# Performance work log

Measured on AMD Instinct MI355X. Metric: run time of the kernel, lower is better.

The kernel has to match this reference:

```python
import jax, jax.numpy as jnp
import numpy as np

VOCAB = 50000
COVOCAB = 50000
D = 300
NUM_SENSES = 4
B = 100000


def _xavier(key, shape):
    fan_in, fan_out = shape[-2], shape[-1]
    if len(shape) == 3:
        fan_in, fan_out = shape[1], shape[2]
    limit = (6.0 / (fan_in + fan_out)) ** 0.5
    return jax.random.uniform(key, shape, jnp.float32, -limit, limit)


def setup_inputs() -> dict:
    key = jax.random.key(0)
    k1, k2, k3, k4, k5 = jax.random.split(key, 5)
    V = _xavier(k1, (VOCAB, D, NUM_SENSES))
    W = _xavier(k2, (COVOCAB, D, NUM_SENSES))
    vb = _xavier(k3, (VOCAB, NUM_SENSES))
    wb = _xavier(k4, (COVOCAB, NUM_SENSES))
    IJ = jax.random.randint(k5, (B, 2), 0, VOCAB, dtype=jnp.int64)
    return {"V": V, "W": W, "vb": vb, "wb": wb, "IJ": IJ}


def reference(V, W, vb, wb, IJ):
    i = IJ[:, 0]
    j = IJ[:, 1]
    Vg = V[i]            # [B, d, s_v]  gather
    Wg = W[j]            # [B, d, s_w]  gather
    # bmm(W[j]^T, V[i]) -> [B, s_w, s_v]
    mat = jnp.einsum("bds,bdt->bst", Wg, Vg)
    bias = wb[j][:, :, None] + vb[i][:, None, :]   # [B, s_w, s_v]
    mat = mat + bias
    # faithful to original: log(sum(exp(.)))
    return jnp.log(jnp.sum(jnp.exp(mat), axis=(1, 2)))
```

## Files before the change

kernel.cpp:

```cpp
#include <hip/hip_runtime.h>
#include <hip/hip_bf16.h>


constexpr int D   = 300;
constexpr int NS  = 4;
constexpr int ROW = D * NS;

__global__ __launch_bounds__(256) void multisense_kernel(
    const float* __restrict__ V,
    const float* __restrict__ W,
    const float* __restrict__ vb,
    const float* __restrict__ wb,
    const unsigned int* __restrict__ IJw,
    float* __restrict__ out,
    int B)
{
    const int lane = threadIdx.x & 63;
    const int b    = blockIdx.x * (blockDim.x >> 6) + (threadIdx.x >> 6);
    if (b >= B) return;

    unsigned int probe = (lane < 32) ? IJw[2 * lane + 1] : 0u;
    const bool isI64 = (__ballot(probe != 0u) == 0ull);

    int i, j;
    if (isI64) { i = (int)IJw[4 * (size_t)b];     j = (int)IJw[4 * (size_t)b + 2]; }
    else       { i = (int)IJw[2 * (size_t)b];     j = (int)IJw[2 * (size_t)b + 1]; }

    const float* __restrict__ Vr = V + (size_t)i * ROW;
    const float* __restrict__ Wr = W + (size_t)j * ROW;

    const int s_idx = (lane >> 4) & 3;
    const int t_idx = (lane >> 2) & 3;

    const float wbj = wb[(size_t)j * NS + s_idx];
    const float vbi = vb[(size_t)i * NS + t_idx];

    float4 va[5], wa[5];
#pragma unroll
    for (int k = 0; k < 4; ++k) {
        const int d = lane + 64 * k;
        va[k] = *reinterpret_cast<const float4*>(Vr + (size_t)d * NS);
        wa[k] = *reinterpret_cast<const float4*>(Wr + (size_t)d * NS);
    }
    {
        const int  d4 = 256 + lane;
        const int  dc = (d4 < D) ? d4 : 0;
        const float m = (d4 < D) ? 1.0f : 0.0f;
        va[4] = *reinterpret_cast<const float4*>(Vr + (size_t)dc * NS);
        wa[4] = *reinterpret_cast<const float4*>(Wr + (size_t)dc * NS);
        wa[4].x *= m; wa[4].y *= m; wa[4].z *= m; wa[4].w *= m;
    }

    float acc[16];
#pragma unroll
    for (int m = 0; m < 16; ++m) acc[m] = 0.0f;
#pragma unroll
    for (int k = 0; k < 5; ++k) {
        const float v0 = va[k].x, v1 = va[k].y, v2 = va[k].z, v3 = va[k].w;
        const float w0 = wa[k].x, w1 = wa[k].y, w2 = wa[k].z, w3 = wa[k].w;
        acc[ 0] = fmaf(w0, v0, acc[ 0]); acc[ 1] = fmaf(w0, v1, acc[ 1]);
        acc[ 2] = fmaf(w0, v2, acc[ 2]); acc[ 3] = fmaf(w0, v3, acc[ 3]);
        acc[ 4] = fmaf(w1, v0, acc[ 4]); acc[ 5] = fmaf(w1, v1, acc[ 5]);
        acc[ 6] = fmaf(w1, v2, acc[ 6]); acc[ 7] = fmaf(w1, v3, acc[ 7]);
        acc[ 8] = fmaf(w2, v0, acc[ 8]); acc[ 9] = fmaf(w2, v1, acc[ 9]);
        acc[10] = fmaf(w2, v2, acc[10]); acc[11] = fmaf(w2, v3, acc[11]);
        acc[12] = fmaf(w3, v0, acc[12]); acc[13] = fmaf(w3, v1, acc[13]);
        acc[14] = fmaf(w3, v2, acc[14]); acc[15] = fmaf(w3, v3, acc[15]);
    }

    const bool b5 = (lane & 32) != 0;
    float r8[8];
#pragma unroll
    for (int m = 0; m < 8; ++m) {
        const float send = b5 ? acc[m]     : acc[m + 8];
        const float keep = b5 ? acc[m + 8] : acc[m];
        r8[m] = keep + __shfl_xor(send, 32, 64);
    }
    const bool b4 = (lane & 16) != 0;
    float r4[4];
#pragma unroll
    for (int m = 0; m < 4; ++m) {
        const float send = b4 ? r8[m]     : r8[m + 4];
        const float keep = b4 ? r8[m + 4] : r8[m];
        r4[m] = keep + __shfl_xor(send, 16, 64);
    }
    const bool b3 = (lane & 8) != 0;
    float r2[2];
#pragma unroll
    for (int m = 0; m < 2; ++m) {
        const float send = b3 ? r4[m]     : r4[m + 2];
        const float keep = b3 ? r4[m + 2] : r4[m];
        r2[m] = keep + __shfl_xor(send, 8, 64);
    }
    const bool b2 = (lane & 4) != 0;
    float r1;
    {
        const float send = b2 ? r2[0] : r2[1];
        const float keep = b2 ? r2[1] : r2[0];
        r1 = keep + __shfl_xor(send, 4, 64);
    }
    r1 += __shfl_xor(r1, 2, 64);
    r1 += __shfl_xor(r1, 1, 64);

    float e = expf(r1 + wbj + vbi);
    e += __shfl_xor(e,  4, 64);
    e += __shfl_xor(e,  8, 64);
    e += __shfl_xor(e, 16, 64);
    e += __shfl_xor(e, 32, 64);

    if (lane == 0) out[b] = logf(e);
}

extern "C" void kernel_launch(void* const* d_in, const int* in_sizes, int n_in,
                              void* d_out, int out_size, void* d_ws, size_t ws_size,
                              hipStream_t stream) {
    const float* V  = (const float*)d_in[0];
    const float* W  = (const float*)d_in[1];
    const float* vb = (const float*)d_in[2];
    const float* wb = (const float*)d_in[3];
    const unsigned int* IJ = (const unsigned int*)d_in[4];
    float* out = (float*)d_out;

    const int B = out_size;
    const int wavesPerBlock = 4;
    dim3 block(256);
    dim3 grid((B + wavesPerBlock - 1) / wavesPerBlock);
    hipLaunchKernelGGL(multisense_kernel, grid, block, 0, stream,
                       V, W, vb, wb, IJ, out, B);
}
```

Baseline: 510.4 us.

## Software-pipeline gathers with persistent waves and inline-asm double-buffered loads

Replaces the one-wave-per-row launch with a persistent grid of 1024 blocks, where each wave walks rows with a grid stride. Each wave prefetches the next row's V/W slices, biases and the index pair after next into a second register set while it computes the current row. Explicit vmcnt waits and sched barriers hold this order. The goal is to hide gather latency, which matters because each row is latency-bound with little work, at the cost of more registers and fragile hand-counted waitcnts. It also picks the index width on the host from the input size instead of probing.

```diff
diff --git a/kernel.cpp b/kernel.cpp
--- a/kernel.cpp
+++ b/kernel.cpp
@@ -1,10 +1,102 @@
 #include <hip/hip_runtime.h>
-#include <hip/hip_bf16.h>
-
-
-constexpr int D   = 300;
-constexpr int NS  = 4;
-constexpr int ROW = D * NS;
+
+
+typedef __attribute__((ext_vector_type(4))) float f32x4;
+
+constexpr int D    = 300;
+constexpr int NS   = 4;
+constexpr int ROWB = D * NS * 4;
+
+#define S_VMCNT(N) asm volatile("s_waitcnt vmcnt(" #N ")" ::: "memory")
+
+#define STAGE(NV, NW, pV_, pW_, pVt_, pWt_)                                                  \
+    asm volatile("global_load_dwordx4 %0, %1, off"             : "=v"(NV[0]) : "v"(pV_));    \
+    asm volatile("global_load_dwordx4 %0, %1, off offset:1024" : "=v"(NV[1]) : "v"(pV_));    \
+    asm volatile("global_load_dwordx4 %0, %1, off offset:2048" : "=v"(NV[2]) : "v"(pV_));    \
+    asm volatile("global_load_dwordx4 %0, %1, off offset:3072" : "=v"(NV[3]) : "v"(pV_));    \
+    asm volatile("global_load_dwordx4 %0, %1, off"             : "=v"(NV[4]) : "v"(pVt_));   \
+    asm volatile("global_load_dwordx4 %0, %1, off"             : "=v"(NW[0]) : "v"(pW_));    \
+    asm volatile("global_load_dwordx4 %0, %1, off offset:1024" : "=v"(NW[1]) : "v"(pW_));    \
+    asm volatile("global_load_dwordx4 %0, %1, off offset:2048" : "=v"(NW[2]) : "v"(pW_));    \
+    asm volatile("global_load_dwordx4 %0, %1, off offset:3072" : "=v"(NW[3]) : "v"(pW_));    \
+    asm volatile("global_load_dwordx4 %0, %1, off"             : "=v"(NW[4]) : "v"(pWt_));
+
+#define COMPUTE(CV, CW, WBC, VBC)                                                            \
+  {                                                                                          \
+    float acc[16];                                                                           \
+    { const float v0=CV[0].x, v1=CV[0].y, v2=CV[0].z, v3=CV[0].w;                            \
+      const float w0=CW[0].x, w1=CW[0].y, w2=CW[0].z, w3=CW[0].w;                            \
+      acc[ 0]=w0*v0; acc[ 1]=w0*v1; acc[ 2]=w0*v2; acc[ 3]=w0*v3;                            \
+      acc[ 4]=w1*v0; acc[ 5]=w1*v1; acc[ 6]=w1*v2; acc[ 7]=w1*v3;                            \
+      acc[ 8]=w2*v0; acc[ 9]=w2*v1; acc[10]=w2*v2; acc[11]=w2*v3;                            \
+      acc[12]=w3*v0; acc[13]=w3*v1; acc[14]=w3*v2; acc[15]=w3*v3; }                          \
+    _Pragma("unroll")                                                                        \
+    for (int k = 1; k < 5; ++k) {                                                            \
+      f32x4 vv = CV[k]; f32x4 ww = CW[k];                                                    \
+      if (k == 4) { ww.x*=mT; ww.y*=mT; ww.z*=mT; ww.w*=mT; }                                \
+      const float v0=vv.x, v1=vv.y, v2=vv.z, v3=vv.w;                                        \
+      const float w0=ww.x, w1=ww.y, w2=ww.z, w3=ww.w;                                        \
+      acc[ 0]=fmaf(w0,v0,acc[ 0]); acc[ 1]=fmaf(w0,v1,acc[ 1]);                              \
+      acc[ 2]=fmaf(w0,v2,acc[ 2]); acc[ 3]=fmaf(w0,v3,acc[ 3]);                              \
+      acc[ 4]=fmaf(w1,v0,acc[ 4]); acc[ 5]=fmaf(w1,v1,acc[ 5]);                              \
+      acc[ 6]=fmaf(w1,v2,acc[ 6]); acc[ 7]=fmaf(w1,v3,acc[ 7]);                              \
+      acc[ 8]=fmaf(w2,v0,acc[ 8]); acc[ 9]=fmaf(w2,v1,acc[ 9]);                              \
+      acc[10]=fmaf(w2,v2,acc[10]); acc[11]=fmaf(w2,v3,acc[11]);                              \
+      acc[12]=fmaf(w3,v0,acc[12]); acc[13]=fmaf(w3,v1,acc[13]);                              \
+      acc[14]=fmaf(w3,v2,acc[14]); acc[15]=fmaf(w3,v3,acc[15]); }                            \
+    float r8[8];                                                                             \
+    _Pragma("unroll")                                                                        \
+    for (int mm = 0; mm < 8; ++mm) {                                                         \
+      const float send = b5 ? acc[mm]     : acc[mm + 8];                                     \
+      const float keep = b5 ? acc[mm + 8] : acc[mm];                                         \
+      r8[mm] = keep + __shfl_xor(send, 32, 64); }                                            \
+    float r4[4];                                                                             \
+    _Pragma("unroll")                                                                        \
+    for (int mm = 0; mm < 4; ++mm) {                                                         \
+      const float send = b4_ ? r8[mm]     : r8[mm + 4];                                      \
+      const float keep = b4_ ? r8[mm + 4] : r8[mm];                                          \
+      r4[mm] = keep + __shfl_xor(send, 16, 64); }                                            \
+    float r2[2];                                                                             \
+    _Pragma("unroll")                                                                        \
+    for (int mm = 0; mm < 2; ++mm) {                                                         \
+      const float send = b3 ? r4[mm]     : r4[mm + 2];                                       \
+      const float keep = b3 ? r4[mm + 2] : r4[mm];                                           \
+      r2[mm] = keep + __shfl_xor(send, 8, 64); }                                             \
+    float r1;                                                                                \
+    { const float send = b2 ? r2[0] : r2[1];                                                 \
+      const float keep = b2 ? r2[1] : r2[0];                                                 \
+      r1 = keep + __shfl_xor(send, 4, 64); }                                                 \
+    r1 += __shfl_xor(r1, 2, 64);                                                             \
+    r1 += __shfl_xor(r1, 1, 64);                                                             \
+    float ex = expf(r1 + (WBC) + (VBC));                                                     \
+    ex += __shfl_xor(ex,  4, 64);                                                            \
+    ex += __shfl_xor(ex,  8, 64);                                                            \
+    ex += __shfl_xor(ex, 16, 64);                                                            \
+    ex += __shfl_xor(ex, 32, 64);                                                            \
+    if (lane == 0) out[e] = logf(ex);                                                        \
+  }
+
+#define STEP(CV, CW, WBC, VBC, IJI, IJJ, NV, NW, WBN, VBN, IJI2, IJJ2)                       \
+  {                                                                                          \
+    S_VMCNT(12); __builtin_amdgcn_sched_barrier(0);                                          \
+    const int iN = (int)(IJI), jN = (int)(IJJ);                                              \
+    const int eNN = (eNext + stride < B) ? (eNext + stride) : (B - 1);                       \
+    { const char* pI_ = ijb + (size_t)eNN * ijstride;                                        \
+      asm volatile("global_load_dword %0, %1, off" : "=v"(IJI2) : "v"(pI_));                 \
+      asm volatile("global_load_dword %0, %1, off" : "=v"(IJJ2) : "v"(pI_ + ijoff)); }       \
+    { const char* pV_  = (const char*)V + (size_t)iN * ROWB + laneB;                         \
+      const char* pW_  = (const char*)W + (size_t)jN * ROWB + laneB;                         \
+      const char* pVt_ = (const char*)V + (size_t)iN * ROWB + dcb;                           \
+      const char* pWt_ = (const char*)W + (size_t)jN * ROWB + dcb;                           \
+      STAGE(NV, NW, pV_, pW_, pVt_, pWt_);                                                   \
+      const char* pwb_ = (const char*)wb + (size_t)jN * 16 + s4;                             \
+      const char* pvb_ = (const char*)vb + (size_t)iN * 16 + t4;                             \
+      asm volatile("global_load_dword %0, %1, off" : "=v"(WBN) : "v"(pwb_));                 \
+      asm volatile("global_load_dword %0, %1, off" : "=v"(VBN) : "v"(pvb_)); }               \
+    S_VMCNT(14); __builtin_amdgcn_sched_barrier(0);                                          \
+    COMPUTE(CV, CW, WBC, VBC);                                                               \
+    e = eNext; eNext = eNN;                                                                  \
+  }
 
 __global__ __launch_bounds__(256) void multisense_kernel(
     const float* __restrict__ V,
@@ -13,102 +105,72 @@
     const float* __restrict__ wb,
     const unsigned int* __restrict__ IJw,
     float* __restrict__ out,
-    int B)
+    int B,
+    int mode,
+    int stride)
 {
     const int lane = threadIdx.x & 63;
-    const int b    = blockIdx.x * (blockDim.x >> 6) + (threadIdx.x >> 6);
-    if (b >= B) return;
-
-    unsigned int probe = (lane < 32) ? IJw[2 * lane + 1] : 0u;
-    const bool isI64 = (__ballot(probe != 0u) == 0ull);
-
-    int i, j;
-    if (isI64) { i = (int)IJw[4 * (size_t)b];     j = (int)IJw[4 * (size_t)b + 2]; }
-    else       { i = (int)IJw[2 * (size_t)b];     j = (int)IJw[2 * (size_t)b + 1]; }
-
-    const float* __restrict__ Vr = V + (size_t)i * ROW;
-    const float* __restrict__ Wr = W + (size_t)j * ROW;
-
-    const int s_idx = (lane >> 4) & 3;
-    const int t_idx = (lane >> 2) & 3;
-
-    const float wbj = wb[(size_t)j * NS + s_idx];
-    const float vbi = vb[(size_t)i * NS + t_idx];
-
-    float4 va[5], wa[5];
-#pragma unroll
-    for (int k = 0; k < 4; ++k) {
-        const int d = lane + 64 * k;
-        va[k] = *reinterpret_cast<const float4*>(Vr + (size_t)d * NS);
-        wa[k] = *reinterpret_cast<const float4*>(Wr + (size_t)d * NS);
+    const int wid  = blockIdx.x * (blockDim.x >> 6) + (threadIdx.x >> 6);
+    int e = wid;
+    if (e >= B) return;
+
+    size_t ijstride, ijoff;
+    if (mode == 1)      { ijstride = 16; ijoff = 8; }
+    else if (mode == 2) { ijstride = 8;  ijoff = 4; }
+    else {
+        unsigned int probe = (lane < 32) ? IJw[2 * lane + 1] : 0u;
+        const bool isI64 = (__ballot(probe != 0u) == 0ull);
+        ijstride = isI64 ? 16 : 8;  ijoff = isI64 ? 8 : 4;
     }
+    const char* ijb = (const char*)IJw;
+
+    const int    s_idx = (lane >> 4) & 3;
+    const int    t_idx = (lane >> 2) & 3;
+    const size_t s4    = (size_t)s_idx * 4;
+    const size_t t4    = (size_t)t_idx * 4;
+    const int    laneB = lane * 16;
+    const int    d4    = 256 + lane;
+    const size_t dcb   = (size_t)((d4 < D) ? d4 : 0) * 16;
+    const float  mT    = (d4 < D) ? 1.0f : 0.0f;
+    const bool   b5  = (lane & 32) != 0;
+    const bool   b4_ = (lane & 16) != 0;
+    const bool   b3  = (lane & 8)  != 0;
+    const bool   b2  = (lane & 4)  != 0;
+
+    const int n = 1 + (B - 1 - e) / stride;
+
+    f32x4 vA[5], wA[5], vB_[5], wB_[5];
+    float wbA, vbA, wbB, vbB;
+    unsigned int ijiA, ijjA, ijiB, ijjB;
+
+    { const char* pI = ijb + (size_t)e * ijstride;
+      asm volatile("global_load_dword %0, %1, off" : "=v"(ijiB) : "v"(pI));
+      asm volatile("global_load_dword %0, %1, off" : "=v"(ijjB) : "v"(pI + ijoff)); }
+    S_VMCNT(0); __builtin_amdgcn_sched_barrier(0);
+    int eNext = (e + stride < B) ? (e + stride) : (B - 1);
     {
-        const int  d4 = 256 + lane;
-        const int  dc = (d4 < D) ? d4 : 0;
-        const float m = (d4 < D) ? 1.0f : 0.0f;
-        va[4] = *reinterpret_cast<const float4*>(Vr + (size_t)dc * NS);
-        wa[4] = *reinterpret_cast<const float4*>(Wr + (size_t)dc * NS);
-        wa[4].x *= m; wa[4].y *= m; wa[4].z *= m; wa[4].w *= m;
+        const int i0 = (int)ijiB, j0 = (int)ijjB;
+        const char* pI = ijb + (size_t)eNext * ijstride;
+        asm volatile("global_load_dword %0, %1, off" : "=v"(ijiB) : "v"(pI));
+        asm volatile("global_load_dword %0, %1, off" : "=v"(ijjB) : "v"(pI + ijoff));
+        const char* pV  = (const char*)V + (size_t)i0 * ROWB + laneB;
+        const char* pW  = (const char*)W + (size_t)j0 * ROWB + laneB;
+        const char* pVt = (const char*)V + (size_t)i0 * ROWB + dcb;
+        const char* pWt = (const char*)W + (size_t)j0 * ROWB + dcb;
+        STAGE(vA, wA, pV, pW, pVt, pWt);
+        const char* pwb = (const char*)wb + (size_t)j0 * 16 + s4;
+        const char* pvb = (const char*)vb + (size_t)i0 * 16 + t4;
+        asm volatile("global_load_dword %0, %1, off" : "=v"(wbA) : "v"(pwb));
+        asm volatile("global_load_dword %0, %1, off" : "=v"(vbA) : "v"(pvb));
     }
 
-    float acc[16];
-#pragma unroll
-    for (int m = 0; m < 16; ++m) acc[m] = 0.0f;
-#pragma unroll
-    for (int k = 0; k < 5; ++k) {
-        const float v0 = va[k].x, v1 = va[k].y, v2 = va[k].z, v3 = va[k].w;
-        const float w0 = wa[k].x, w1 = wa[k].y, w2 = wa[k].z, w3 = wa[k].w;
-        acc[ 0] = fmaf(w0, v0, acc[ 0]); acc[ 1] = fmaf(w0, v1, acc[ 1]);
-        acc[ 2] = fmaf(w0, v2, acc[ 2]); acc[ 3] = fmaf(w0, v3, acc[ 3]);
-        acc[ 4] = fmaf(w1, v0, acc[ 4]); acc[ 5] = fmaf(w1, v1, acc[ 5]);
-        acc[ 6] = fmaf(w1, v2, acc[ 6]); acc[ 7] = fmaf(w1, v3, acc[ 7]);
-        acc[ 8] = fmaf(w2, v0, acc[ 8]); acc[ 9] = fmaf(w2, v1, acc[ 9]);
-        acc[10] = fmaf(w2, v2, acc[10]); acc[11] = fmaf(w2, v3, acc[11]);
-        acc[12] = fmaf(w3, v0, acc[12]); acc[13] = fmaf(w3, v1, acc[13]);
-        acc[14] = fmaf(w3, v2, acc[14]); acc[15] = fmaf(w3, v3, acc[15]);
+    int rem = n;
+    for (;;) {
+        STEP(vA,  wA,  wbA, vbA, ijiB, ijjB, vB_, wB_, wbB, vbB, ijiA, ijjA);
+        if (--rem == 0) break;
+        STEP(vB_, wB_, wbB, vbB, ijiA, ijjA, vA,  wA,  wbA, vbA, ijiB, ijjB);
+        if (--rem == 0) break;
     }
-
-    const bool b5 = (lane & 32) != 0;
-    float r8[8];
-#pragma unroll
-    for (int m = 0; m < 8; ++m) {
-        const float send = b5 ? acc[m]     : acc[m + 8];
-        const float keep = b5 ? acc[m + 8] : acc[m];
-        r8[m] = keep + __shfl_xor(send, 32, 64);
-    }
-    const bool b4 = (lane & 16) != 0;
-    float r4[4];
-#pragma unroll
-    for (int m = 0; m < 4; ++m) {
-        const float send = b4 ? r8[m]     : r8[m + 4];
-        const float keep = b4 ? r8[m + 4] : r8[m];
-        r4[m] = keep + __shfl_xor(send, 16, 64);
-    }
-    const bool b3 = (lane & 8) != 0;
-    float r2[2];
-#pragma unroll
-    for (int m = 0; m < 2; ++m) {
-        const float send = b3 ? r4[m]     : r4[m + 2];
-        const float keep = b3 ? r4[m + 2] : r4[m];
-        r2[m] = keep + __shfl_xor(send, 8, 64);
-    }
-    const bool b2 = (lane & 4) != 0;
-    float r1;
-    {
-        const float send = b2 ? r2[0] : r2[1];
-        const float keep = b2 ? r2[1] : r2[0];
-        r1 = keep + __shfl_xor(send, 4, 64);
-    }
-    r1 += __shfl_xor(r1, 2, 64);
-    r1 += __shfl_xor(r1, 1, 64);
-
-    float e = expf(r1 + wbj + vbi);
-    e += __shfl_xor(e,  4, 64);
-    e += __shfl_xor(e,  8, 64);
-    e += __shfl_xor(e, 16, 64);
-    e += __shfl_xor(e, 32, 64);
-
-    if (lane == 0) out[b] = logf(e);
 }
 
 extern "C" void kernel_launch(void* const* d_in, const int* in_sizes, int n_in,
@@ -122,9 +184,20 @@
     float* out = (float*)d_out;
 
     const int B = out_size;
+
+    int mode = 0;
+    const long long szIJ = (long long)in_sizes[4];
+    if      (szIJ == (long long)B * 16) mode = 1;
+    else if (szIJ == (long long)B * 8)  mode = 2;
+
     const int wavesPerBlock = 4;
+    int blocks = 1024;
+    const int maxBlocks = (B + wavesPerBlock - 1) / wavesPerBlock;
+    if (blocks > maxBlocks) blocks = maxBlocks;
+    const int stride = blocks * wavesPerBlock;
+
     dim3 block(256);
-    dim3 grid((B + wavesPerBlock - 1) / wavesPerBlock);
+    dim3 grid(blocks);
     hipLaunchKernelGGL(multisense_kernel, grid, block, 0, stream,
-                       V, W, vb, wb, IJ, out, B);
+                       V, W, vb, wb, IJ, out, B, mode, stride);
 }
```

Measured after the change: 512.5 us. About the same (+0.4%).
